# Optimization experiments

Hardware: AMD Instinct MI355X
Metric: run time of the kernel (lower is better)

Reference implementation:

```python
import jax, jax.numpy as jnp
import numpy as np

B, C, IN_DIM, OUT_DIM, H = 8, 2048, 128, 128, 4
D = OUT_DIM // H  # d_k = 32


def setup_inputs() -> dict:
    key = jax.random.key(0)
    ks = jax.random.split(key, 7)
    s = 1.0 / np.sqrt(IN_DIM)
    x = jax.random.normal(ks[0], (B, C, IN_DIM), dtype=jnp.float32)
    adj = jax.random.uniform(ks[1], (B, C, C), dtype=jnp.float32)
    Wq = jax.random.uniform(ks[2], (IN_DIM, H * D), jnp.float32, -s, s)
    Wk = jax.random.uniform(ks[3], (IN_DIM, H * D), jnp.float32, -s, s)
    Wv = jax.random.uniform(ks[4], (IN_DIM, H * D), jnp.float32, -s, s)
    so = 1.0 / np.sqrt(H * D)
    Wo = jax.random.uniform(ks[5], (H * D, OUT_DIM), jnp.float32, -so, so)
    bo = jax.random.uniform(ks[6], (OUT_DIM,), jnp.float32, -so, so)
    return {"x": x, "adj": adj, "Wq": Wq, "Wk": Wk, "Wv": Wv, "Wo": Wo, "bo": bo}


def reference(x, adj, Wq, Wk, Wv, Wo, bo):
    # Project to per-head Q/K/V: (B, H, C, D)
    def proj(W):
        return (x @ W).reshape(B, C, H, D).transpose(0, 2, 1, 3)
    Q, K, V = proj(Wq), proj(Wk), proj(Wv)
    # Scaled dot-product scores, adjacency-gated, LeakyReLU(0.2), softmax
    scores = jnp.einsum('bhqd,bhkd->bhqk', Q, K) / jnp.sqrt(jnp.float32(D))
    scores = scores * adj[:, None, :, :]
    scores = jnp.where(scores > 0, scores, 0.2 * scores)  # LeakyReLU(0.2)
    attn = jax.nn.softmax(scores, axis=-1)  # dropout is identity at eval
    out = jnp.einsum('bhqk,bhkd->bhqd', attn, V)
    out = out.transpose(0, 2, 1, 3).reshape(B, C, H * D)  # concat heads
    return out @ Wo + bo
```

## Files before the change

### kernel.cpp

```cpp
#include <hip/hip_runtime.h>
#include <hip/hip_bf16.h>

constexpr int B_  = 8;
constexpr int C_  = 2048;
constexpr int IND = 128;
constexpr int H_  = 4;
constexpr int D_  = 32;
constexpr int M_  = B_ * C_;
constexpr float QSCALE = 0.17677669529663687f;
constexpr float L2E    = 1.4426950408889634f;
constexpr float QL2    = QSCALE * L2E;

constexpr int KSPLIT = 4;
constexpr int KPG = C_ / KSPLIT;

typedef __attribute__((ext_vector_type(8))) short short8;
typedef __attribute__((ext_vector_type(4))) short s4t;
typedef __attribute__((ext_vector_type(4))) float f4t;
typedef __attribute__((ext_vector_type(4))) unsigned short us4;

#if __has_builtin(__builtin_amdgcn_mfma_f32_16x16x16bf16_1k)
#define MFMA16(a, b, c) __builtin_amdgcn_mfma_f32_16x16x16bf16_1k(a, b, c, 0, 0, 0)
#else
#define MFMA16(a, b, c) (c)
#endif
#define MFMA32(a, b, c) __builtin_amdgcn_mfma_f32_16x16x32_bf16(a, b, c, 0, 0, 0)

__device__ __forceinline__ unsigned short f2bf(float f) {
    union { float f; unsigned u; } v; v.f = f;
    unsigned u = v.u + 0x7fffu + ((v.u >> 16) & 1u);
    return (unsigned short)(u >> 16);
}

__device__ __forceinline__ s4t pack4_bf16(float p0, float p1, float p2, float p3) {
#if __has_builtin(__builtin_amdgcn_cvt_pk_bf16_f32)
    auto a = __builtin_amdgcn_cvt_pk_bf16_f32(p0, p1);
    auto b = __builtin_amdgcn_cvt_pk_bf16_f32(p2, p3);
    unsigned u[2];
    __builtin_memcpy(&u[0], &a, 4);
    __builtin_memcpy(&u[1], &b, 4);
    s4t pp;
    __builtin_memcpy(&pp, u, 8);
    return pp;
#else
    s4t pp;
    pp[0] = (short)f2bf(p0); pp[1] = (short)f2bf(p1);
    pp[2] = (short)f2bf(p2); pp[3] = (short)f2bf(p3);
    return pp;
#endif
}

__device__ __forceinline__ short8 cvt8(float4 a, float4 b) {
    s4t x = pack4_bf16(a.x, a.y, a.z, a.w);
    s4t y = pack4_bf16(b.x, b.y, b.z, b.w);
    short8 r;
    r[0] = x[0]; r[1] = x[1]; r[2] = x[2]; r[3] = x[3];
    r[4] = y[0]; r[5] = y[1]; r[6] = y[2]; r[7] = y[3];
    return r;
}

__global__ __launch_bounds__(256) void prep_w_kernel(
    const float* __restrict__ Wq, const float* __restrict__ Wk,
    const float* __restrict__ Wv, const float* __restrict__ Wo,
    unsigned short* __restrict__ Wtb)
{
    __shared__ unsigned short lds[16][130];
    const int t  = threadIdx.x;
    const int n0 = blockIdx.x * 16;

    const float* src; int nb; float sc = 1.0f;
    if      (n0 < 128) { src = Wq; nb = n0;       sc = QL2; }
    else if (n0 < 256) { src = Wk; nb = n0 - 128; }
    else if (n0 < 384) { src = Wv; nb = n0 - 256; }
    else               { src = Wo; nb = n0 - 384; }

    const int nn = t & 15, kk = t >> 4;
#pragma unroll
    for (int kb = 0; kb < 8; ++kb) {
        const int k = kb * 16 + kk;
        lds[nn][k] = f2bf(src[k * IND + nb + nn] * sc);
    }
    __syncthreads();
    const int k = t & 127, rr = t >> 7;
#pragma unroll
    for (int it = 0; it < 8; ++it) {
        const int r = it * 2 + rr;
        Wtb[(size_t)(n0 + r) * IND + k] = lds[r][k];
    }
}

__global__ __launch_bounds__(192) void qkv_proj_kernel(
    const float* __restrict__ x, const unsigned short* __restrict__ Wtb,
    unsigned short* __restrict__ Qb, unsigned short* __restrict__ Kb,
    unsigned short* __restrict__ Vt)
{
    const int t = threadIdx.x;
    const int w = t >> 6;
    const int l = t & 63;
    const int lo = l & 15, hi = l >> 4;
    const int tok0 = blockIdx.x * 16;
    const int b  = tok0 >> 11;
    const int cb = tok0 & 2047;
    const int tile0 = blockIdx.y * 4;

    short8 xb[4];
    const float* xrow = x + (size_t)(tok0 + lo) * IND;
#pragma unroll
    for (int kc = 0; kc < 4; ++kc) {
        const float4 a = *(const float4*)(xrow + kc * 32 + hi * 8);
        const float4 c = *(const float4*)(xrow + kc * 32 + hi * 8 + 4);
        xb[kc] = cvt8(a, c);
    }

    const unsigned short* wbase = Wtb + (size_t)(w * 128) * IND;
#pragma unroll
    for (int tile = 0; tile < 4; ++tile) {
        const int n0 = (tile0 + tile) * 16;
        short8 wf[4];
#pragma unroll
        for (int kc = 0; kc < 4; ++kc)
            wf[kc] = *(const short8*)(wbase + (size_t)(n0 + lo) * IND +
                                      kc * 32 + hi * 8);
        f4t acc = 0.f;
        if (w < 2) {
#pragma unroll
            for (int kc = 0; kc < 4; ++kc) acc = MFMA32(wf[kc], xb[kc], acc);
            us4 v;
#pragma unroll
            for (int r = 0; r < 4; ++r) v[r] = f2bf(acc[r]);
            unsigned short* O = (w == 0) ? Qb : Kb;
            *(us4*)(O + (size_t)(tok0 + lo) * IND + n0 + hi * 4) = v;
        } else {
#pragma unroll
            for (int kc = 0; kc < 4; ++kc) acc = MFMA32(xb[kc], wf[kc], acc);
            us4 v;
#pragma unroll
            for (int r = 0; r < 4; ++r) v[r] = f2bf(acc[r]);
            *(us4*)(Vt + ((size_t)(b * IND) + n0 + lo) * C_ + cb + hi * 4) = v;
        }
    }
}

__global__ __launch_bounds__(256, 4) void attn_kernel(
    const unsigned short* __restrict__ Qb, const unsigned short* __restrict__ Kb,
    const unsigned short* __restrict__ Vt, const float* __restrict__ adj,
    float* __restrict__ Opart, float* __restrict__ lpart)
{
    __shared__ __align__(16) char Ksm[3][4096];
    __shared__ __align__(16) char Vsm[3][4096];
    __shared__ __align__(16) char Asm[3][4096];

    const int t  = threadIdx.x;
    const int s  = t >> 6;
    const int l  = t & 63;
    const int lo = l & 15, hi = l >> 4;
    const int b  = blockIdx.y;
    const int kz = blockIdx.z;
    const int q0 = blockIdx.x * 64;
    const int qs = q0 + s * 16 + lo;
    const int kzoff = kz * KPG;
    const int NCH = KPG / 16;

    const int keyS = s * 4 + (l >> 4);
    const char* srcK = (const char*)Kb + ((size_t)(b * C_ + kzoff) + keyS) * 256
                       + (((l & 15) * 16) ^ ((keyS & 7) << 4));
    const int dS = s * 32 + (l >> 1);
    const char* srcV = (const char*)Vt + (size_t)(b * IND + dS) * (C_ * 2)
                       + (size_t)kzoff * 2 + (l & 1) * 16;
    const int qS = s * 16 + (l >> 2);
    const char* srcA = (const char*)adj
                       + ((size_t)(b * C_ + q0 + qS) * C_ + kzoff) * 4
                       + (l & 3) * 16;

#if __has_builtin(__builtin_amdgcn_global_load_lds)
#define GLL(gp, lp) __builtin_amdgcn_global_load_lds( \
    (const __attribute__((address_space(1))) unsigned int*)(gp), \
    (__attribute__((address_space(3))) unsigned int*)(lp), 16, 0, 0)
#else
#define GLL(gp, lp) (void)(gp)
#endif

    auto stage = [&](int c, int buf) {
        GLL(srcK + (size_t)c * 4096, Ksm[buf] + s * 1024);
        GLL(srcV + (size_t)c * 32,   Vsm[buf] + s * 1024);
        GLL(srcA + (size_t)c * 64,   Asm[buf] + s * 1024);
    };

    short8 qf[4];
#pragma unroll
    for (int h = 0; h < 4; ++h)
        qf[h] = *(const short8*)(Qb + ((size_t)(b * C_) + qs) * IND + h * 32 + hi * 8);
    __builtin_amdgcn_sched_barrier(0);
    stage(0, 0);
    __builtin_amdgcn_sched_barrier(0);
    stage(1, 1);
    __builtin_amdgcn_sched_barrier(0);

    f4t acc[4][2];
#pragma unroll
    for (int h = 0; h < 4; ++h) { acc[h][0] = 0.f; acc[h][1] = 0.f; }
    float ls[4] = {0.f, 0.f, 0.f, 0.f};

    const int x7 = (lo & 7) << 4;

    auto computeC = [&](int buf) {
        const char* Kl = Ksm[buf];
        const char* Vl = Vsm[buf];
        const char* Al = Asm[buf];
        short8 kf[4];
#pragma unroll
        for (int h = 0; h < 4; ++h)
            kf[h] = *(const short8*)(Kl + lo * 256 + ((h * 64 + hi * 16) ^ x7));
        s4t vf[8];
#pragma unroll
        for (int h = 0; h < 4; ++h) {
            vf[h * 2]     = *(const s4t*)(Vl + (h * 32 + lo) * 32 + hi * 8);
            vf[h * 2 + 1] = *(const s4t*)(Vl + (h * 32 + 16 + lo) * 32 + hi * 8);
        }
        const f4t av = *(const f4t*)(Al + (s * 16 + lo) * 64 + hi * 16);
#pragma unroll
        for (int h = 0; h < 4; ++h) {
            f4t st4 = MFMA32(kf[h], qf[h], (f4t)0.f);
            float p[4];
#pragma unroll
            for (int r = 0; r < 4; ++r) {
                const float a = st4[r] * av[r];
                const float m = fmaxf(a, 0.2f * a);
                p[r] = exp2f(m);
                ls[h] += p[r];
            }
            const s4t pp = pack4_bf16(p[0], p[1], p[2], p[3]);
            acc[h][0] = MFMA16(pp, vf[h * 2], acc[h][0]);
            acc[h][1] = MFMA16(pp, vf[h * 2 + 1], acc[h][1]);
        }
    };

    int bc = 0, bn = 1, bs = 2;
    for (int c = 0; c < NCH; ++c) {
        if (c + 1 < NCH) { asm volatile("s_waitcnt vmcnt(3)" ::: "memory"); }
        else             { asm volatile("s_waitcnt vmcnt(0)" ::: "memory"); }
        __builtin_amdgcn_sched_barrier(0);
        __builtin_amdgcn_s_barrier();
        __builtin_amdgcn_sched_barrier(0);

        if (c + 2 < NCH) stage(c + 2, bs);
        computeC(bc);

        const int tmp = bc; bc = bn; bn = bs; bs = tmp;
    }

#pragma unroll
    for (int h = 0; h < 4; ++h) {
        ls[h] += __shfl_xor(ls[h], 16, 64);
        ls[h] += __shfl_xor(ls[h], 32, 64);
    }

    const size_t BHC   = (size_t)B_ * H_ * C_;
    const size_t obase = (size_t)kz * BHC;

    const float lw = (hi == 0) ? ls[0] : (hi == 1) ? ls[1] : (hi == 2) ? ls[2] : ls[3];
    lpart[obase + (size_t)(b * H_ + hi) * C_ + qs] = lw;

#pragma unroll
    for (int h = 0; h < 4; ++h) {
        const size_t rb = obase + (size_t)(b * H_ + h) * C_ + q0 + s * 16 + hi * 4;
#pragma unroll
        for (int dh = 0; dh < 2; ++dh)
#pragma unroll
            for (int r = 0; r < 4; ++r)
                Opart[(rb + r) * D_ + dh * 16 + lo] = acc[h][dh][r];
    }
#undef GLL
}

__global__ __launch_bounds__(256) void out_proj_kernel(
    const float* __restrict__ Opart, const float* __restrict__ lpart,
    const unsigned short* __restrict__ Wtb, const float* __restrict__ bo,
    float* __restrict__ out)
{
    __shared__ __align__(16) char AOsm[4096];

    const int t  = threadIdx.x;
    const int w  = t >> 6;
    const int l  = t & 63;
    const int lo = l & 15, hi = l >> 4;
    const int tok0 = blockIdx.x * 16;
    const int b  = tok0 >> 11;
    const int q0 = tok0 & 2047;
    const size_t BHC = (size_t)B_ * H_ * C_;

    {
        const int ra = l >> 3;
        const int dq = l & 7;
        float4 va = {0.f, 0.f, 0.f, 0.f}, vb = {0.f, 0.f, 0.f, 0.f};
        float la = 0.f, lb = 0.f;
#pragma unroll
        for (int kz = 0; kz < KSPLIT; ++kz) {
            const size_t rowb = (size_t)kz * BHC + (size_t)(b * H_ + w) * C_ + q0;
            la += lpart[rowb + ra];
            lb += lpart[rowb + ra + 8];
            const float* R = Opart + rowb * D_;
            const float4 u = *(const float4*)(R + l * 4);
            const float4 v = *(const float4*)(R + 256 + l * 4);
            va.x += u.x; va.y += u.y; va.z += u.z; va.w += u.w;
            vb.x += v.x; vb.y += v.y; vb.z += v.z; vb.w += v.w;
        }
        const float ia = 1.f / la, ib = 1.f / lb;
        const s4t pa = pack4_bf16(va.x * ia, va.y * ia, va.z * ia, va.w * ia);
        const s4t pb = pack4_bf16(vb.x * ib, vb.y * ib, vb.z * ib, vb.w * ib);
        const int colb = w * 64 + dq * 8;
        *(s4t*)(AOsm + ra * 256       + (colb ^ ((ra & 7) << 4))) = pa;
        *(s4t*)(AOsm + (ra + 8) * 256 + (colb ^ ((ra & 7) << 4))) = pb;
    }
    __syncthreads();

    short8 af[4];
#pragma unroll
    for (int kc = 0; kc < 4; ++kc)
        af[kc] = *(const short8*)(AOsm + lo * 256 +
                                  ((kc * 64 + hi * 16) ^ ((lo & 7) << 4)));

    const unsigned short* wbase = Wtb + (size_t)384 * IND;
#pragma unroll
    for (int tt = 0; tt < 2; ++tt) {
        const int n0 = w * 32 + tt * 16;
        short8 wf[4];
#pragma unroll
        for (int kc = 0; kc < 4; ++kc)
            wf[kc] = *(const short8*)(wbase + (size_t)(n0 + lo) * IND +
                                      kc * 32 + hi * 8);
        f4t acc = 0.f;
#pragma unroll
        for (int kc = 0; kc < 4; ++kc) acc = MFMA32(wf[kc], af[kc], acc);
        const f4t bv = *(const f4t*)(bo + n0 + hi * 4);
        float4 o;
        o.x = acc[0] + bv[0]; o.y = acc[1] + bv[1];
        o.z = acc[2] + bv[2]; o.w = acc[3] + bv[3];
        *(float4*)(out + (size_t)(tok0 + lo) * IND + n0 + hi * 4) = o;
    }
}

extern "C" void kernel_launch(void* const* d_in, const int* in_sizes, int n_in,
                              void* d_out, int out_size, void* d_ws, size_t ws_size,
                              hipStream_t stream) {
    const float* x   = (const float*)d_in[0];
    const float* adj = (const float*)d_in[1];
    const float* Wq  = (const float*)d_in[2];
    const float* Wk  = (const float*)d_in[3];
    const float* Wv  = (const float*)d_in[4];
    const float* Wo  = (const float*)d_in[5];
    const float* bo  = (const float*)d_in[6];
    float* out = (float*)d_out;

    unsigned short* Wtb = (unsigned short*)d_ws;
    unsigned short* Qb  = Wtb + (size_t)512 * IND;
    unsigned short* Kb  = Qb + (size_t)M_ * IND;
    unsigned short* Vt  = Kb + (size_t)M_ * IND;
    unsigned short* AOb = Vt + (size_t)M_ * IND;
    float* Opart = (float*)(AOb + (size_t)M_ * IND);
    float* lpart = Opart + (size_t)KSPLIT * B_ * H_ * C_ * D_;

    hipLaunchKernelGGL(prep_w_kernel, dim3(32), dim3(256), 0, stream,
                       Wq, Wk, Wv, Wo, Wtb);
    hipLaunchKernelGGL(qkv_proj_kernel, dim3(M_ / 16, 2), dim3(192), 0, stream,
                       x, Wtb, Qb, Kb, Vt);
    hipLaunchKernelGGL(attn_kernel, dim3(C_ / 64, B_, KSPLIT), dim3(256), 0, stream,
                       Qb, Kb, Vt, adj, Opart, lpart);
    hipLaunchKernelGGL(out_proj_kernel, dim3(M_ / 16), dim3(256), 0, stream,
                       Opart, lpart, Wtb, bo, out);
}
```

Before: 285.5 us.

## Split heads across wave pairs and shrink attention tile to 32 queries

Each attention block now covers 32 queries instead of 64, and pairs of waves split the four heads, so each wave handles 16 queries and two heads. Staging drops from triple to double buffering with an extra barrier before each refill, and only two waves load the smaller adjacency tile. The per-block register and LDS footprint shrinks to allow more resident blocks (launch bounds raised to 7). The cost is that K and V tiles are reloaded for twice as many blocks, and each chunk now needs an extra barrier with less prefetch depth.

Measured after the change: 306.5 us. +7.3%, slower.

```diff
diff --git a/kernel.cpp b/kernel.cpp
--- a/kernel.cpp
+++ b/kernel.cpp
@@ -141,33 +141,35 @@
     }
 }
 
-__global__ __launch_bounds__(256, 4) void attn_kernel(
+__global__ __launch_bounds__(256, 7) void attn_kernel(
     const unsigned short* __restrict__ Qb, const unsigned short* __restrict__ Kb,
     const unsigned short* __restrict__ Vt, const float* __restrict__ adj,
     float* __restrict__ Opart, float* __restrict__ lpart)
 {
-    __shared__ __align__(16) char Ksm[3][4096];
-    __shared__ __align__(16) char Vsm[3][4096];
-    __shared__ __align__(16) char Asm[3][4096];
+    __shared__ __align__(16) char Ksm[2][4096];
+    __shared__ __align__(16) char Vsm[2][4096];
+    __shared__ __align__(16) char Asm[2][2048];
 
     const int t  = threadIdx.x;
-    const int s  = t >> 6;
+    const int w  = t >> 6;
+    const int s2 = w >> 1;
+    const int hh = w & 1;
     const int l  = t & 63;
     const int lo = l & 15, hi = l >> 4;
     const int b  = blockIdx.y;
     const int kz = blockIdx.z;
-    const int q0 = blockIdx.x * 64;
-    const int qs = q0 + s * 16 + lo;
+    const int q0 = blockIdx.x * 32;
+    const int qs = q0 + s2 * 16 + lo;
     const int kzoff = kz * KPG;
     const int NCH = KPG / 16;
 
-    const int keyS = s * 4 + (l >> 4);
+    const int keyS = w * 4 + (l >> 4);
     const char* srcK = (const char*)Kb + ((size_t)(b * C_ + kzoff) + keyS) * 256
                        + (((l & 15) * 16) ^ ((keyS & 7) << 4));
-    const int dS = s * 32 + (l >> 1);
+    const int dS = w * 32 + (l >> 1);
     const char* srcV = (const char*)Vt + (size_t)(b * IND + dS) * (C_ * 2)
                        + (size_t)kzoff * 2 + (l & 1) * 16;
-    const int qS = s * 16 + (l >> 2);
+    const int qS = (w & 1) * 16 + (l >> 2);
     const char* srcA = (const char*)adj
                        + ((size_t)(b * C_ + q0 + qS) * C_ + kzoff) * 4
                        + (l & 3) * 16;
@@ -181,25 +183,27 @@
 #endif
 
     auto stage = [&](int c, int buf) {
-        GLL(srcK + (size_t)c * 4096, Ksm[buf] + s * 1024);
-        GLL(srcV + (size_t)c * 32,   Vsm[buf] + s * 1024);
-        GLL(srcA + (size_t)c * 64,   Asm[buf] + s * 1024);
+        GLL(srcK + (size_t)c * 4096, Ksm[buf] + w * 1024);
+        GLL(srcV + (size_t)c * 32,   Vsm[buf] + w * 1024);
+        if (w < 2)
+            GLL(srcA + (size_t)c * 64, Asm[buf] + w * 1024);
     };
 
-    short8 qf[4];
-#pragma unroll
-    for (int h = 0; h < 4; ++h)
-        qf[h] = *(const short8*)(Qb + ((size_t)(b * C_) + qs) * IND + h * 32 + hi * 8);
+    short8 qf[2];
+#pragma unroll
+    for (int h = 0; h < 2; ++h)
+        qf[h] = *(const short8*)(Qb + ((size_t)(b * C_) + qs) * IND +
+                                 (hh * 2 + h) * 32 + hi * 8);
     __builtin_amdgcn_sched_barrier(0);
     stage(0, 0);
     __builtin_amdgcn_sched_barrier(0);
     stage(1, 1);
     __builtin_amdgcn_sched_barrier(0);
 
-    f4t acc[4][2];
-#pragma unroll
-    for (int h = 0; h < 4; ++h) { acc[h][0] = 0.f; acc[h][1] = 0.f; }
-    float ls[4] = {0.f, 0.f, 0.f, 0.f};
+    f4t acc[2][2];
+#pragma unroll
+    for (int h = 0; h < 2; ++h) { acc[h][0] = 0.f; acc[h][1] = 0.f; }
+    float ls[2] = {0.f, 0.f};
 
     const int x7 = (lo & 7) << 4;
 
@@ -207,19 +211,21 @@
         const char* Kl = Ksm[buf];
         const char* Vl = Vsm[buf];
         const char* Al = Asm[buf];
-        short8 kf[4];
-#pragma unroll
-        for (int h = 0; h < 4; ++h)
-            kf[h] = *(const short8*)(Kl + lo * 256 + ((h * 64 + hi * 16) ^ x7));
-        s4t vf[8];
-#pragma unroll
-        for (int h = 0; h < 4; ++h) {
-            vf[h * 2]     = *(const s4t*)(Vl + (h * 32 + lo) * 32 + hi * 8);
-            vf[h * 2 + 1] = *(const s4t*)(Vl + (h * 32 + 16 + lo) * 32 + hi * 8);
-        }
-        const f4t av = *(const f4t*)(Al + (s * 16 + lo) * 64 + hi * 16);
-#pragma unroll
-        for (int h = 0; h < 4; ++h) {
+        short8 kf[2];
+#pragma unroll
+        for (int h = 0; h < 2; ++h)
+            kf[h] = *(const short8*)(Kl + lo * 256 +
+                                     (((hh * 2 + h) * 64 + hi * 16) ^ x7));
+        s4t vf[4];
+#pragma unroll
+        for (int h = 0; h < 2; ++h) {
+            const int g = hh * 2 + h;
+            vf[h * 2]     = *(const s4t*)(Vl + (g * 32 + lo) * 32 + hi * 8);
+            vf[h * 2 + 1] = *(const s4t*)(Vl + (g * 32 + 16 + lo) * 32 + hi * 8);
+        }
+        const f4t av = *(const f4t*)(Al + (s2 * 16 + lo) * 64 + hi * 16);
+#pragma unroll
+        for (int h = 0; h < 2; ++h) {
             f4t st4 = MFMA32(kf[h], qf[h], (f4t)0.f);
             float p[4];
 #pragma unroll
@@ -235,22 +241,28 @@
         }
     };
 
-    int bc = 0, bn = 1, bs = 2;
     for (int c = 0; c < NCH; ++c) {
-        if (c + 1 < NCH) { asm volatile("s_waitcnt vmcnt(3)" ::: "memory"); }
-        else             { asm volatile("s_waitcnt vmcnt(0)" ::: "memory"); }
+        if (c + 1 < NCH) {
+            if (w < 2) { asm volatile("s_waitcnt vmcnt(3)" ::: "memory"); }
+            else       { asm volatile("s_waitcnt vmcnt(2)" ::: "memory"); }
+        } else {
+            asm volatile("s_waitcnt vmcnt(0)" ::: "memory");
+        }
         __builtin_amdgcn_sched_barrier(0);
         __builtin_amdgcn_s_barrier();
         __builtin_amdgcn_sched_barrier(0);
 
-        if (c + 2 < NCH) stage(c + 2, bs);
-        computeC(bc);
-
-        const int tmp = bc; bc = bn; bn = bs; bs = tmp;
-    }
-
-#pragma unroll
-    for (int h = 0; h < 4; ++h) {
+        computeC(c & 1);
+
+        asm volatile("s_waitcnt lgkmcnt(0)" ::: "memory");
+        __builtin_amdgcn_sched_barrier(0);
+        __builtin_amdgcn_s_barrier();
+        __builtin_amdgcn_sched_barrier(0);
+        if (c + 2 < NCH) stage(c + 2, c & 1);
+    }
+
+#pragma unroll
+    for (int h = 0; h < 2; ++h) {
         ls[h] += __shfl_xor(ls[h], 16, 64);
         ls[h] += __shfl_xor(ls[h], 32, 64);
     }
@@ -258,12 +270,15 @@
     const size_t BHC   = (size_t)B_ * H_ * C_;
     const size_t obase = (size_t)kz * BHC;
 
-    const float lw = (hi == 0) ? ls[0] : (hi == 1) ? ls[1] : (hi == 2) ? ls[2] : ls[3];
-    lpart[obase + (size_t)(b * H_ + hi) * C_ + qs] = lw;
-
-#pragma unroll
-    for (int h = 0; h < 4; ++h) {
-        const size_t rb = obase + (size_t)(b * H_ + h) * C_ + q0 + s * 16 + hi * 4;
+    if (hi < 2) {
+        const float lw = (hi == 0) ? ls[0] : ls[1];
+        lpart[obase + (size_t)(b * H_ + hh * 2 + hi) * C_ + qs] = lw;
+    }
+
+#pragma unroll
+    for (int h = 0; h < 2; ++h) {
+        const int g = hh * 2 + h;
+        const size_t rb = obase + (size_t)(b * H_ + g) * C_ + q0 + s2 * 16 + hi * 4;
 #pragma unroll
         for (int dh = 0; dh < 2; ++dh)
 #pragma unroll
@@ -364,7 +379,7 @@
                        Wq, Wk, Wv, Wo, Wtb);
     hipLaunchKernelGGL(qkv_proj_kernel, dim3(M_ / 16, 2), dim3(192), 0, stream,
                        x, Wtb, Qb, Kb, Vt);
-    hipLaunchKernelGGL(attn_kernel, dim3(C_ / 64, B_, KSPLIT), dim3(256), 0, stream,
+    hipLaunchKernelGGL(attn_kernel, dim3(C_ / 32, B_, KSPLIT), dim3(256), 0, stream,
                        Qb, Kb, Vt, adj, Opart, lpart);
     hipLaunchKernelGGL(out_proj_kernel, dim3(M_ / 16), dim3(256), 0, stream,
                        Opart, lpart, Wtb, bo, out);
```
